# Optimization experiments

Measured on AMD Instinct MI355X. Metric: run time of the kernel, lower is better.

Reference implementation:

```python
import jax, jax.numpy as jnp
import numpy as np

N = 4_194_304  # nodes along the plane element
EPS = 1e-8


def setup_inputs() -> dict:
    key = jax.random.key(0)
    k0, = jax.random.split(key, 1)
    depth = jax.random.uniform(k0, (N,), jnp.float32) * 0.05  # initial surface depth [m]
    return dict(
        depth=depth,
        rain_rate=jnp.float32(2.8e-5),   # ~100 mm/hr
        dt=jnp.float32(1.0),             # s
        cum_rain=jnp.float32(0.01),      # m (bookkeeping input)
        theta_current=jnp.float32(0.25),
        F_cumulative=jnp.float32(0.002),
        WID=jnp.float32(1.0),
        SS1=jnp.float32(1.0),
        SS2=jnp.float32(1.0),
        MAN=jnp.float32(0.03),
        SL=jnp.float32(0.01),
        dx=jnp.float32(1.0),
        Ks=jnp.float32(1.0e-6),
        psi=jnp.float32(0.11),
        theta_s=jnp.float32(0.45),
    )


def _manning_q(A, WID, SS1, SS2, MAN, SL):
    # trapezoid wetted perimeter from plane depth h = A / WID
    h = A / WID
    wp = WID + h * (jnp.sqrt(1.0 + SS1 * SS1) + jnp.sqrt(1.0 + SS2 * SS2))
    A_safe = jnp.maximum(A, EPS)
    return A * (A_safe / wp) ** (2.0 / 3.0) * jnp.sqrt(SL) / MAN


def _minmod(a, b):
    return jnp.where(a * b > 0.0, jnp.where(jnp.abs(a) < jnp.abs(b), a, b), 0.0)


def reference(depth, rain_rate, dt, cum_rain, theta_current, F_cumulative,
              WID, SS1, SS2, MAN, SL, dx, Ks, psi, theta_s):
    # --- Green-Ampt infiltration per node (surface head as extra driving head) ---
    dtheta = jnp.maximum(theta_s - theta_current, 0.0)
    F_safe = jnp.maximum(F_cumulative, 1e-6)
    fp = Ks * (1.0 + (psi * dtheta + depth) / F_safe)   # potential rate [m/s], [N]
    avail = rain_rate * dt + depth                      # available water this step [m]
    infil_depth_nodes = jnp.minimum(fp * dt, avail)     # [N]
    infil_rate_nodes = infil_depth_nodes / dt

    # --- rain-depth add + clamp, area from depth ---
    surf = jnp.maximum(depth + rain_rate * dt - infil_depth_nodes, 0.0)
    A = surf * WID                                      # [N]

    # --- explicit MUSCL kinematic-wave update (minmod limiter, upwind flux) ---
    dA = jnp.diff(A)                                    # [N-1]
    zero = jnp.zeros((1,), A.dtype)
    slope = jnp.concatenate([zero, _minmod(dA[:-1], dA[1:]), zero])  # [N]
    A_face = A + 0.5 * slope                            # left state at face i+1/2
    flux = _manning_q(A_face, WID, SS1, SS2, MAN, SL)   # outgoing flux per node [N]
    flux_in = jnp.concatenate([zero, flux[:-1]])        # upstream_Q = 0 at inlet
    A_next = jnp.maximum(A - (dt / dx) * (flux - flux_in), 0.0)

    # --- Manning discharge on updated state ---
    Q = _manning_q(A_next, WID, SS1, SS2, MAN, SL)      # [N]
    outflow_q = Q[-1]

    # --- CFL reduction ---
    vel = Q / jnp.maximum(A_next, EPS)
    max_cfl = jnp.max(vel * dt / dx)

    infil_rate_element = jnp.mean(infil_rate_nodes)
    infil_depth_element = jnp.mean(infil_depth_nodes)
    return outflow_q, infil_rate_element, infil_depth_element, max_cfl
```

## Files before the change

### kernel.cpp

```cpp
#include <hip/hip_runtime.h>

#define EPSF 1e-8f

__device__ __forceinline__ float minmodf(float a, float b) {
    return (a * b > 0.0f) ? (fabsf(a) < fabsf(b) ? a : b) : 0.0f;
}

__device__ __forceinline__ float pow23(float x) {
    return __expf(0.66666667f * __logf(x));
}

__device__ __forceinline__ float manning_q(float A, float WID, float invWID,
                                           float s12, float coef) {
    float wp = WID + (A * invWID) * s12;
    float As = fmaxf(A, EPSF);
    return A * pow23(__fdividef(As, wp)) * coef;
}

__device__ __forceinline__ float area_from_depth(float d, float Ks, float KsF,
                                                 float pdt, float dt, float raindt,
                                                 float WID, float* infil_out) {
    float fp    = Ks + KsF * (pdt + d);
    float infil = fminf(fp * dt, raindt + d);
    float surf  = fmaxf(d + raindt - infil, 0.0f);
    *infil_out  = infil;
    return surf * WID;
}

__global__ __launch_bounds__(256) void plane_element_kernel(
    const float* __restrict__ depth,
    const float* __restrict__ s_rain, const float* __restrict__ s_dt,
    const float* __restrict__ s_theta, const float* __restrict__ s_F,
    const float* __restrict__ s_WID, const float* __restrict__ s_SS1,
    const float* __restrict__ s_SS2, const float* __restrict__ s_MAN,
    const float* __restrict__ s_SL, const float* __restrict__ s_dx,
    const float* __restrict__ s_Ks, const float* __restrict__ s_psi,
    const float* __restrict__ s_thetas,
    float* __restrict__ out,
    float* __restrict__ ws_sum, float* __restrict__ ws_max, int N) {

    const float rain = *s_rain, dt = *s_dt, theta_c = *s_theta, Fc = *s_F;
    const float WID = *s_WID, SS1 = *s_SS1, SS2 = *s_SS2, MAN = *s_MAN;
    const float SL = *s_SL, dx = *s_dx, Ks = *s_Ks, psi = *s_psi, ths = *s_thetas;

    const float dtheta = fmaxf(ths - theta_c, 0.0f);
    const float F_safe = fmaxf(Fc, 1e-6f);
    const float KsF    = Ks / F_safe;
    const float pdt    = psi * dtheta;
    const float raindt = rain * dt;
    const float s12    = sqrtf(1.0f + SS1 * SS1) + sqrtf(1.0f + SS2 * SS2);
    const float coef   = sqrtf(SL) / MAN;
    const float invWID = 1.0f / WID;
    const float r      = dt / dx;

    float sum_infil = 0.0f;
    float maxcfl    = 0.0f;
    float infil, dump;

    const int nchunks = N >> 3;
    const int stride  = gridDim.x * blockDim.x;

    for (int c = blockIdx.x * blockDim.x + threadIdx.x; c < nchunks; c += stride) {
        const int base = c << 3;

        float d[11];
        if (base >= 2) {
            const float2 t = *(const float2*)(depth + base - 2);
            d[0] = t.x; d[1] = t.y;
        } else {
            d[0] = d[1] = depth[0];
        }
        const float4 m0 = *(const float4*)(depth + base);
        const float4 m1 = *(const float4*)(depth + base + 4);
        d[2] = m0.x; d[3] = m0.y; d[4] = m0.z; d[5] = m0.w;
        d[6] = m1.x; d[7] = m1.y; d[8] = m1.z; d[9] = m1.w;
        d[10] = (base + 8 < N) ? depth[base + 8] : 0.0f;

        const float a_m2 = area_from_depth(d[0], Ks, KsF, pdt, dt, raindt, WID, &dump);
        float a_im1      = area_from_depth(d[1], Ks, KsF, pdt, dt, raindt, WID, &dump);
        float a_i        = area_from_depth(d[2], Ks, KsF, pdt, dt, raindt, WID, &infil);
        sum_infil += infil;

        float f_prev = 0.0f;
        if (base > 0) {
            const float sl = minmodf(a_im1 - a_m2, a_i - a_im1);
            f_prev = manning_q(a_im1 + 0.5f * sl, WID, invWID, s12, coef);
        }

#pragma unroll
        for (int j = 0; j < 8; ++j) {
            const int i = base + j;
            const float a_ip1 =
                area_from_depth(d[3 + j], Ks, KsF, pdt, dt, raindt, WID, &infil);
            if (j < 7) sum_infil += infil;

            const float sl = (i == 0 || i == N - 1)
                                 ? 0.0f
                                 : minmodf(a_i - a_im1, a_ip1 - a_i);
            const float flux_i = manning_q(a_i + 0.5f * sl, WID, invWID, s12, coef);
            const float fin    = (i == 0) ? 0.0f : f_prev;

            const float An  = fmaxf(a_i - r * (flux_i - fin), 0.0f);
            const float Qi  = manning_q(An, WID, invWID, s12, coef);
            const float vel = __fdividef(Qi, fmaxf(An, EPSF));
            maxcfl          = fmaxf(maxcfl, vel * r);

            if (i == N - 1) out[0] = Qi;

            f_prev = flux_i;
            a_im1  = a_i;
            a_i    = a_ip1;
        }
    }

    for (int off = 32; off > 0; off >>= 1) {
        sum_infil += __shfl_down(sum_infil, off, 64);
        maxcfl     = fmaxf(maxcfl, __shfl_down(maxcfl, off, 64));
    }

    __shared__ float s_sum[4];
    __shared__ float s_max[4];
    const int lane = threadIdx.x & 63;
    const int wave = threadIdx.x >> 6;
    if (lane == 0) { s_sum[wave] = sum_infil; s_max[wave] = maxcfl; }
    __syncthreads();

    if (threadIdx.x == 0) {
        ws_sum[blockIdx.x] = s_sum[0] + s_sum[1] + s_sum[2] + s_sum[3];
        ws_max[blockIdx.x] = fmaxf(fmaxf(s_max[0], s_max[1]),
                                   fmaxf(s_max[2], s_max[3]));
    }
}

__global__ __launch_bounds__(256) void reduce_kernel(
    const float* __restrict__ ws_sum, const float* __restrict__ ws_max,
    const float* __restrict__ s_dt, float* __restrict__ out,
    int nparts, int N) {

    float sum = 0.0f, mx = 0.0f;
    for (int i = threadIdx.x; i < nparts; i += 256) {
        sum += ws_sum[i];
        mx   = fmaxf(mx, ws_max[i]);
    }

    for (int off = 32; off > 0; off >>= 1) {
        sum += __shfl_down(sum, off, 64);
        mx   = fmaxf(mx, __shfl_down(mx, off, 64));
    }

    __shared__ float s_sum[4];
    __shared__ float s_max[4];
    const int lane = threadIdx.x & 63;
    const int wave = threadIdx.x >> 6;
    if (lane == 0) { s_sum[wave] = sum; s_max[wave] = mx; }
    __syncthreads();

    if (threadIdx.x == 0) {
        const float dt   = *s_dt;
        const float mean = (s_sum[0] + s_sum[1] + s_sum[2] + s_sum[3]) / (float)N;
        out[2] = mean;
        out[1] = mean / dt;
        out[3] = fmaxf(fmaxf(s_max[0], s_max[1]), fmaxf(s_max[2], s_max[3]));
    }
}

extern "C" void kernel_launch(void* const* d_in, const int* in_sizes, int n_in,
                              void* d_out, int out_size, void* d_ws, size_t ws_size,
                              hipStream_t stream) {
    const float* depth    = (const float*)d_in[0];
    const float* s_rain   = (const float*)d_in[1];
    const float* s_dt     = (const float*)d_in[2];
    const float* s_theta  = (const float*)d_in[4];
    const float* s_F      = (const float*)d_in[5];
    const float* s_WID    = (const float*)d_in[6];
    const float* s_SS1    = (const float*)d_in[7];
    const float* s_SS2    = (const float*)d_in[8];
    const float* s_MAN    = (const float*)d_in[9];
    const float* s_SL     = (const float*)d_in[10];
    const float* s_dx     = (const float*)d_in[11];
    const float* s_Ks     = (const float*)d_in[12];
    const float* s_psi    = (const float*)d_in[13];
    const float* s_thetas = (const float*)d_in[14];

    float* out = (float*)d_out;
    const int N = in_sizes[0];

    const int block = 256;
    int grid = ((N >> 3) + block - 1) / block;
    if (grid > 2048) grid = 2048;

    float* ws_sum = (float*)d_ws;
    float* ws_max = ws_sum + grid;

    plane_element_kernel<<<grid, block, 0, stream>>>(
        depth, s_rain, s_dt, s_theta, s_F, s_WID, s_SS1, s_SS2, s_MAN,
        s_SL, s_dx, s_Ks, s_psi, s_thetas, out, ws_sum, ws_max, N);

    reduce_kernel<<<1, block, 0, stream>>>(ws_sum, ws_max, s_dt, out, grid, N);
}
```

Baseline: 100.9 us.

## Fuse final reduction into main kernel via cooperative grid sync

Replaces the separate single-block reduce kernel with a cooperative launch that does a grid-wide sync, after which block 0 reduces the per-block partials. The grid is fixed at 1024 blocks and the launch bounds now request 4 blocks per CU so all blocks can be co-resident. The per-node CFL velocity now reuses the Manning factor, dropping one divide per node. The cooperative launch and grid barrier add their own overhead, and the fixed grid size may change load balance.

```diff
diff --git a/kernel.cpp b/kernel.cpp
--- a/kernel.cpp
+++ b/kernel.cpp
@@ -1,4 +1,7 @@
 #include <hip/hip_runtime.h>
+#include <hip/hip_cooperative_groups.h>
+
+namespace cg = cooperative_groups;
 
 #define EPSF 1e-8f
 
@@ -27,7 +30,7 @@
     return surf * WID;
 }
 
-__global__ __launch_bounds__(256) void plane_element_kernel(
+__global__ __launch_bounds__(256, 4) void plane_element_kernel(
     const float* __restrict__ depth,
     const float* __restrict__ s_rain, const float* __restrict__ s_dt,
     const float* __restrict__ s_theta, const float* __restrict__ s_F,
@@ -101,11 +104,13 @@
             const float fin    = (i == 0) ? 0.0f : f_prev;
 
             const float An  = fmaxf(a_i - r * (flux_i - fin), 0.0f);
-            const float Qi  = manning_q(An, WID, invWID, s12, coef);
-            const float vel = __fdividef(Qi, fmaxf(An, EPSF));
+            const float wp  = WID + (An * invWID) * s12;
+            const float As  = fmaxf(An, EPSF);
+            const float p   = pow23(__fdividef(As, wp)) * coef;
+            const float vel = p * fminf(An * 1e8f, 1.0f);
             maxcfl          = fmaxf(maxcfl, vel * r);
 
-            if (i == N - 1) out[0] = Qi;
+            if (i == N - 1) out[0] = An * p;
 
             f_prev = flux_i;
             a_im1  = a_i;
@@ -129,38 +134,31 @@
         ws_sum[blockIdx.x] = s_sum[0] + s_sum[1] + s_sum[2] + s_sum[3];
         ws_max[blockIdx.x] = fmaxf(fmaxf(s_max[0], s_max[1]),
                                    fmaxf(s_max[2], s_max[3]));
-    }
-}
-
-__global__ __launch_bounds__(256) void reduce_kernel(
-    const float* __restrict__ ws_sum, const float* __restrict__ ws_max,
-    const float* __restrict__ s_dt, float* __restrict__ out,
-    int nparts, int N) {
-
-    float sum = 0.0f, mx = 0.0f;
-    for (int i = threadIdx.x; i < nparts; i += 256) {
-        sum += ws_sum[i];
-        mx   = fmaxf(mx, ws_max[i]);
-    }
-
-    for (int off = 32; off > 0; off >>= 1) {
-        sum += __shfl_down(sum, off, 64);
-        mx   = fmaxf(mx, __shfl_down(mx, off, 64));
-    }
-
-    __shared__ float s_sum[4];
-    __shared__ float s_max[4];
-    const int lane = threadIdx.x & 63;
-    const int wave = threadIdx.x >> 6;
-    if (lane == 0) { s_sum[wave] = sum; s_max[wave] = mx; }
-    __syncthreads();
-
-    if (threadIdx.x == 0) {
-        const float dt   = *s_dt;
-        const float mean = (s_sum[0] + s_sum[1] + s_sum[2] + s_sum[3]) / (float)N;
-        out[2] = mean;
-        out[1] = mean / dt;
-        out[3] = fmaxf(fmaxf(s_max[0], s_max[1]), fmaxf(s_max[2], s_max[3]));
+        __threadfence();
+    }
+
+    cg::this_grid().sync();
+
+    if (blockIdx.x == 0) {
+        float sum = 0.0f, mx = 0.0f;
+        for (int i = threadIdx.x; i < gridDim.x; i += 256) {
+            sum += ws_sum[i];
+            mx   = fmaxf(mx, ws_max[i]);
+        }
+        for (int off = 32; off > 0; off >>= 1) {
+            sum += __shfl_down(sum, off, 64);
+            mx   = fmaxf(mx, __shfl_down(mx, off, 64));
+        }
+        __shared__ float r_sum[4];
+        __shared__ float r_max[4];
+        if (lane == 0) { r_sum[wave] = sum; r_max[wave] = mx; }
+        __syncthreads();
+        if (threadIdx.x == 0) {
+            const float mean = (r_sum[0] + r_sum[1] + r_sum[2] + r_sum[3]) / (float)N;
+            out[2] = mean;
+            out[1] = mean / dt;
+            out[3] = fmaxf(fmaxf(r_max[0], r_max[1]), fmaxf(r_max[2], r_max[3]));
+        }
     }
 }
 
@@ -183,18 +181,21 @@
     const float* s_thetas = (const float*)d_in[14];
 
     float* out = (float*)d_out;
-    const int N = in_sizes[0];
+    int N = in_sizes[0];
 
     const int block = 256;
-    int grid = ((N >> 3) + block - 1) / block;
-    if (grid > 2048) grid = 2048;
+    const int grid  = 1024;
 
     float* ws_sum = (float*)d_ws;
     float* ws_max = ws_sum + grid;
 
-    plane_element_kernel<<<grid, block, 0, stream>>>(
-        depth, s_rain, s_dt, s_theta, s_F, s_WID, s_SS1, s_SS2, s_MAN,
-        s_SL, s_dx, s_Ks, s_psi, s_thetas, out, ws_sum, ws_max, N);
-
-    reduce_kernel<<<1, block, 0, stream>>>(ws_sum, ws_max, s_dt, out, grid, N);
-}
+    void* args[] = {
+        (void*)&depth,  (void*)&s_rain, (void*)&s_dt,   (void*)&s_theta,
+        (void*)&s_F,    (void*)&s_WID,  (void*)&s_SS1,  (void*)&s_SS2,
+        (void*)&s_MAN,  (void*)&s_SL,   (void*)&s_dx,   (void*)&s_Ks,
+        (void*)&s_psi,  (void*)&s_thetas, (void*)&out,
+        (void*)&ws_sum, (void*)&ws_max, (void*)&N,
+    };
+    hipLaunchCooperativeKernel((const void*)plane_element_kernel,
+                               dim3(grid), dim3(block), args, 0, stream);
+}
```

Measured after the change: 208.0 us. +106.2%, slower.
